# Kernel optimization log

Measured on AMD Instinct MI355X. Metric: run time of the kernel, lower is better.

Reference implementation:

```python
import jax, jax.numpy as jnp
import numpy as np

BETA = 0.9
THRESHOLD = 1.0
SLOPE = 25.0  # snntorch fast_sigmoid default slope


@jax.custom_vjp
def spike_fn(u):
    # Heaviside spike with fast-sigmoid surrogate gradient
    return (u > 0).astype(u.dtype)

def _spike_fwd(u):
    return spike_fn(u), u

def _spike_bwd(u, g):
    return (g / (SLOPE * jnp.abs(u) + 1.0) ** 2,)

spike_fn.defvjp(_spike_fwd, _spike_bwd)


def setup_inputs() -> dict:
    key = jax.random.key(0)
    k1, k2, k3 = jax.random.split(key, 3)
    T, B, D_IN, D_H = 200, 256, 512, 512
    x = jax.random.normal(k1, (T, B, D_IN), dtype=jnp.float32)
    W = jax.random.normal(k2, (D_H, D_IN), dtype=jnp.float32) * (1.0 / np.sqrt(D_IN))
    b = jax.random.normal(k3, (D_H,), dtype=jnp.float32) * 0.01
    return {"x": x, "W": W, "b": b}


def reference(x, W, b):
    # Batch the fc projection over all timesteps: [T,B,D_in] @ [D_in,D_h] -> [T,B,D_h]
    cur = jnp.einsum("tbi,hi->tbh", x, W) + b
    B, H = cur.shape[1], cur.shape[2]
    mem0 = jnp.zeros((B, H), dtype=cur.dtype)

    def step(mem, cur_t):
        # snntorch Leaky (reset_mechanism='subtract'):
        # reset from previous mem, then integrate, then fire
        reset = spike_fn(mem - THRESHOLD)
        mem_new = BETA * mem + cur_t - reset * THRESHOLD
        spk = spike_fn(mem_new - THRESHOLD)
        return mem_new, (spk, mem_new)

    _, (spk_rec, mem_rec) = jax.lax.scan(step, mem0, cur)
    return spk_rec, mem_rec
```

## Files before the change

kernel.cpp:

```cpp
#include <hip/hip_runtime.h>


#define T_STEPS 200
#define BATCH   256
#define DIN     512
#define DH      512
#define MARGIN  1e-4f
#define LISTCAP 510
#define TQ2     32

constexpr int    MM  = T_STEPS * BATCH;
constexpr int    BH  = BATCH * DH;
constexpr size_t TBH = (size_t)T_STEPS * BH;

typedef _Float16 f16x8 __attribute__((ext_vector_type(8)));
typedef _Float16 f16x4 __attribute__((ext_vector_type(4)));
typedef float    f32x4 __attribute__((ext_vector_type(4)));

constexpr size_t OFF_WH    = 104857600;
constexpr size_t OFF_WL    = 105381888;
constexpr size_t OFF_CNTB  = 105906176;
constexpr size_t OFF_LISTB = 105907200;
constexpr size_t WS_REQ    = OFF_LISTB + (size_t)256 * LISTCAP * 4;

__global__ __launch_bounds__(256) void convert_w(const float* __restrict__ W,
                                                 _Float16* __restrict__ wh,
                                                 _Float16* __restrict__ wl) {
    const int q = blockIdx.x * 256 + threadIdx.x;
    const float4 v = reinterpret_cast<const float4*>(W)[q];
    f16x4 h, l;
    h[0] = (_Float16)v.x; l[0] = (_Float16)((v.x - (float)h[0]) * 4096.0f);
    h[1] = (_Float16)v.y; l[1] = (_Float16)((v.y - (float)h[1]) * 4096.0f);
    h[2] = (_Float16)v.z; l[2] = (_Float16)((v.z - (float)h[2]) * 4096.0f);
    h[3] = (_Float16)v.w; l[3] = (_Float16)((v.w - (float)h[3]) * 4096.0f);
    const int row = q >> 7;
    const int k   = (q & 127) * 4;
    const int osw = ((k >> 3) & 3) ^ ((row >> 1) & 3);
    const long long dst = (long long)row * 512 + (k & ~31) + (osw << 3) + (k & 7);
    *reinterpret_cast<f16x4*>(wh + dst) = h;
    *reinterpret_cast<f16x4*>(wl + dst) = l;
}

__device__ __forceinline__ void gload16(const void* g, void* l) {
    __builtin_amdgcn_global_load_lds(
        (const __attribute__((address_space(1))) void*)g,
        (__attribute__((address_space(3))) void*)l, 16, 0, 0);
}

__global__ __launch_bounds__(256) void gemm_split(const float* __restrict__ x,
                                                  const _Float16* __restrict__ wh,
                                                  const _Float16* __restrict__ wl,
                                                  const float* __restrict__ bias,
                                                  float* __restrict__ C) {
    __shared__ _Float16 ldsA[2][2][128][32];
    __shared__ _Float16 ldsB[2][2][64][32];

    const int tid  = threadIdx.x;
    const int w    = tid >> 6;
    const int lane = tid & 63;
    const int wr   = (w >> 1) * 64;
    const int wc   = (w & 1) * 32;
    const int lrow = lane & 15;
    const int gsw  = (((lane >> 4) ^ ((lrow >> 1) & 3)) * 8);

    const int orig = (blockIdx.x & 7) * 400 + (blockIdx.x >> 3);
    const int row0 = (orig >> 3) * 128;
    const int col0 = (orig & 7) * 64;

    const int sr = tid >> 2;
    const int so = tid & 3;
    const int kq = so * 8;

    f32x4 acc_hh[4][2] = {};
    f32x4 acc_cr[4][2] = {};

    auto stage = [&](int bf, int k0) {
#pragma unroll
        for (int p = 0; p < 2; ++p) {
            const int r = sr + p * 64;
            const float* src = &x[(size_t)(row0 + r) * DIN + k0 + kq];
            const float4 v0 = *reinterpret_cast<const float4*>(src);
            const float4 v1 = *reinterpret_cast<const float4*>(src + 4);
            f16x8 h, l;
            h[0] = (_Float16)v0.x; l[0] = (_Float16)((v0.x - (float)h[0]) * 4096.0f);
            h[1] = (_Float16)v0.y; l[1] = (_Float16)((v0.y - (float)h[1]) * 4096.0f);
            h[2] = (_Float16)v0.z; l[2] = (_Float16)((v0.z - (float)h[2]) * 4096.0f);
            h[3] = (_Float16)v0.w; l[3] = (_Float16)((v0.w - (float)h[3]) * 4096.0f);
            h[4] = (_Float16)v1.x; l[4] = (_Float16)((v1.x - (float)h[4]) * 4096.0f);
            h[5] = (_Float16)v1.y; l[5] = (_Float16)((v1.y - (float)h[5]) * 4096.0f);
            h[6] = (_Float16)v1.z; l[6] = (_Float16)((v1.z - (float)h[6]) * 4096.0f);
            h[7] = (_Float16)v1.w; l[7] = (_Float16)((v1.w - (float)h[7]) * 4096.0f);
            const int po = (so ^ ((r >> 1) & 3)) * 8;
            *reinterpret_cast<f16x8*>(&ldsA[bf][0][r][po]) = h;
            *reinterpret_cast<f16x8*>(&ldsA[bf][1][r][po]) = l;
        }
        gload16(wh + (size_t)(col0 + sr) * DIN + k0 + kq, &ldsB[bf][0][sr][kq]);
        gload16(wl + (size_t)(col0 + sr) * DIN + k0 + kq, &ldsB[bf][1][sr][kq]);
    };

    stage(0, 0);

    int buf = 0;
    for (int kt = 0; kt < 16; ++kt) {
        __syncthreads();
        if (kt < 15) stage(buf ^ 1, (kt + 1) * 32);

        f16x8 ah[4], al[4];
#pragma unroll
        for (int fr = 0; fr < 4; ++fr) {
            ah[fr] = *reinterpret_cast<const f16x8*>(&ldsA[buf][0][wr + fr * 16 + lrow][gsw]);
            al[fr] = *reinterpret_cast<const f16x8*>(&ldsA[buf][1][wr + fr * 16 + lrow][gsw]);
        }
#pragma unroll
        for (int fc = 0; fc < 2; ++fc) {
            const f16x8 bh = *reinterpret_cast<const f16x8*>(&ldsB[buf][0][wc + fc * 16 + lrow][gsw]);
            const f16x8 bl = *reinterpret_cast<const f16x8*>(&ldsB[buf][1][wc + fc * 16 + lrow][gsw]);
#pragma unroll
            for (int fr = 0; fr < 4; ++fr) {
                acc_hh[fr][fc] = __builtin_amdgcn_mfma_f32_16x16x32_f16(ah[fr], bh, acc_hh[fr][fc], 0, 0, 0);
                acc_cr[fr][fc] = __builtin_amdgcn_mfma_f32_16x16x32_f16(ah[fr], bl, acc_cr[fr][fc], 0, 0, 0);
                acc_cr[fr][fc] = __builtin_amdgcn_mfma_f32_16x16x32_f16(al[fr], bh, acc_cr[fr][fc], 0, 0, 0);
            }
        }
        buf ^= 1;
    }

#pragma unroll
    for (int fr = 0; fr < 4; ++fr)
#pragma unroll
        for (int fc = 0; fc < 2; ++fc) {
            const int col = col0 + wc + fc * 16 + lrow;
            const float bv = bias[col];
#pragma unroll
            for (int r = 0; r < 4; ++r) {
                const int row = row0 + wr + fr * 16 + (lane >> 4) * 4 + r;
                C[(size_t)row * DH + col] =
                    acc_hh[fr][fc][r] + acc_cr[fr][fc][r] * (1.0f / 4096.0f) + bv;
            }
        }
}

__global__ __launch_bounds__(256) void snn_scan_flag(float* __restrict__ buf,
                                                     float* __restrict__ spk,
                                                     unsigned* __restrict__ cnt_b,
                                                     unsigned* __restrict__ list_b) {
#pragma clang fp contract(off)
    const int i = (blockIdx.x * 256 + threadIdx.x) * 2;
    float2 c[8];
#pragma unroll
    for (int t = 0; t < 8; ++t)
        c[t] = *reinterpret_cast<const float2*>(&buf[(size_t)t * BH + i]);
    float mem0 = 0.0f, mem1 = 0.0f;
    bool f0 = false, f1 = false;
#pragma unroll 8
    for (int t = 0; t < T_STEPS - 8; ++t) {
        const float2 cur = c[t & 7];
        c[t & 7] = *reinterpret_cast<const float2*>(&buf[(size_t)(t + 8) * BH + i]);
        const float r0 = (mem0 > 1.0f) ? 1.0f : 0.0f;
        float tmp0 = 0.9f * mem0; tmp0 = tmp0 + cur.x; mem0 = tmp0 - r0;
        f0 = f0 || (fabsf(mem0 - 1.0f) < MARGIN);
        const float r1 = (mem1 > 1.0f) ? 1.0f : 0.0f;
        float tmp1 = 0.9f * mem1; tmp1 = tmp1 + cur.y; mem1 = tmp1 - r1;
        f1 = f1 || (fabsf(mem1 - 1.0f) < MARGIN);
        float2 s, m;
        s.x = (mem0 > 1.0f) ? 1.0f : 0.0f;
        s.y = (mem1 > 1.0f) ? 1.0f : 0.0f;
        m.x = mem0; m.y = mem1;
        *reinterpret_cast<float2*>(&spk[(size_t)t * BH + i]) = s;
        *reinterpret_cast<float2*>(&buf[(size_t)t * BH + i]) = m;
    }
#pragma unroll
    for (int t = T_STEPS - 8; t < T_STEPS; ++t) {
        const float2 cur = c[t & 7];
        const float r0 = (mem0 > 1.0f) ? 1.0f : 0.0f;
        float tmp0 = 0.9f * mem0; tmp0 = tmp0 + cur.x; mem0 = tmp0 - r0;
        f0 = f0 || (fabsf(mem0 - 1.0f) < MARGIN);
        const float r1 = (mem1 > 1.0f) ? 1.0f : 0.0f;
        float tmp1 = 0.9f * mem1; tmp1 = tmp1 + cur.y; mem1 = tmp1 - r1;
        f1 = f1 || (fabsf(mem1 - 1.0f) < MARGIN);
        float2 s, m;
        s.x = (mem0 > 1.0f) ? 1.0f : 0.0f;
        s.y = (mem1 > 1.0f) ? 1.0f : 0.0f;
        m.x = mem0; m.y = mem1;
        *reinterpret_cast<float2*>(&spk[(size_t)t * BH + i]) = s;
        *reinterpret_cast<float2*>(&buf[(size_t)t * BH + i]) = m;
    }
    if (f0) {
        const int b = i >> 9;
        const unsigned slot = atomicAdd(&cnt_b[b], 1u);
        if (slot < (unsigned)LISTCAP) list_b[(size_t)b * LISTCAP + slot] = (unsigned)(i & 511);
    }
    if (f1) {
        const int b = (i + 1) >> 9;
        const unsigned slot = atomicAdd(&cnt_b[b], 1u);
        if (slot < (unsigned)LISTCAP) list_b[(size_t)b * LISTCAP + slot] = (unsigned)((i + 1) & 511);
    }
}

__global__ __launch_bounds__(256) void exact_cur_g(const float* __restrict__ x,
                                                   const float* __restrict__ W,
                                                   const float* __restrict__ bias,
                                                   const unsigned* __restrict__ cnt_b,
                                                   const unsigned* __restrict__ list_b,
                                                   float* __restrict__ cur_ex) {
    const int b = blockIdx.x;
    unsigned n = cnt_b[b];
    if (n == 0) return;
    const bool all = (n > (unsigned)LISTCAP);
    if (all) n = 512;

    const int jl = (int)(threadIdx.x & 7);
    const int tl = (int)(threadIdx.x >> 3);
    const int t  = blockIdx.y * TQ2 + tl;
    if (t >= T_STEPS) return;
    const float4* xr = reinterpret_cast<const float4*>(x + ((size_t)t * BATCH + b) * DIN);

    for (unsigned base = 0; base < n; base += 8) {
        const unsigned slot = base + (unsigned)jl;
        if (slot >= n) break;
        const int h = all ? (int)slot : (int)list_b[(size_t)b * LISTCAP + slot];
        const float4* wr = reinterpret_cast<const float4*>(W + (size_t)h * DIN);
        float acc = 0.0f;
#pragma unroll 8
        for (int kk = 0; kk < DIN / 4; ++kk) {
            const float4 a = xr[kk];
            const float4 ww = wr[kk];
            acc = fmaf(a.x, ww.x, acc);
            acc = fmaf(a.y, ww.y, acc);
            acc = fmaf(a.z, ww.z, acc);
            acc = fmaf(a.w, ww.w, acc);
        }
        cur_ex[((size_t)b * 512 + slot) * T_STEPS + t] = acc + bias[h];
    }
}

__global__ __launch_bounds__(256) void rescan_g(const float* __restrict__ cur_ex,
                                                const unsigned* __restrict__ cnt_b,
                                                const unsigned* __restrict__ list_b,
                                                float* __restrict__ buf,
                                                float* __restrict__ spk) {
#pragma clang fp contract(off)
    const int b = blockIdx.x;
    unsigned n = cnt_b[b];
    if (n == 0) return;
    const bool all = (n > (unsigned)LISTCAP);
    if (all) n = 512;

    for (unsigned slot = threadIdx.x; slot < n; slot += 256) {
        const int h = all ? (int)slot : (int)list_b[(size_t)b * LISTCAP + slot];
        const unsigned i = ((unsigned)b << 9) | (unsigned)h;
        const float* cr = cur_ex + ((size_t)b * 512 + slot) * T_STEPS;
        float mem = 0.0f;
        for (int t = 0; t < T_STEPS; ++t) {
            const float c = cr[t];
            const float reset = (mem > 1.0f) ? 1.0f : 0.0f;
            float tmp = 0.9f * mem;
            tmp = tmp + c;
            mem = tmp - reset;
            const float s = (mem > 1.0f) ? 1.0f : 0.0f;
            spk[(size_t)t * BH + i] = s;
            buf[(size_t)t * BH + i] = mem;
        }
    }
}

#define BKf 32
#define LPADf 132
__global__ __launch_bounds__(256, 3) void gemm_nt_f32(const float* __restrict__ A,
                                                      const float* __restrict__ W,
                                                      const float* __restrict__ bias,
                                                      float* __restrict__ C) {
    __shared__ float As[BKf][LPADf];
    __shared__ float Bs[BKf][LPADf];
    const int tid = threadIdx.x;
    const int tx = tid & 15, ty = tid >> 4;
    const int row0 = blockIdx.x * 128, col0 = blockIdx.y * 128;
    const int lr = tid >> 2, lk = (tid & 3) * 4;
    const float* Abase = A + (size_t)(row0 + lr) * DIN + lk;
    const float* Bbase = W + (size_t)(col0 + lr) * DIN + lk;
    float acc[8][8] = {};
    float4 ra00, ra01, ra10, ra11, rb00, rb01, rb10, rb11;
#define LOADREG(k0)                                                        \
    do {                                                                   \
        ra00 = *reinterpret_cast<const float4*>(Abase + (k0));             \
        ra01 = *reinterpret_cast<const float4*>(Abase + (k0) + 16);        \
        ra10 = *reinterpret_cast<const float4*>(Abase + 64 * DIN + (k0));  \
        ra11 = *reinterpret_cast<const float4*>(Abase + 64 * DIN + (k0) + 16); \
        rb00 = *reinterpret_cast<const float4*>(Bbase + (k0));             \
        rb01 = *reinterpret_cast<const float4*>(Bbase + (k0) + 16);        \
        rb10 = *reinterpret_cast<const float4*>(Bbase + 64 * DIN + (k0));  \
        rb11 = *reinterpret_cast<const float4*>(Bbase + 64 * DIN + (k0) + 16); \
    } while (0)
#define STOREV(arr, kb, r, v)                                              \
    do { arr[(kb)+0][r]=(v).x; arr[(kb)+1][r]=(v).y; arr[(kb)+2][r]=(v).z; arr[(kb)+3][r]=(v).w; } while (0)
    LOADREG(0);
    for (int kt = 0; kt < DIN / BKf; ++kt) {
        __syncthreads();
        STOREV(As, lk, lr, ra00); STOREV(As, 16 + lk, lr, ra01);
        STOREV(As, lk, lr + 64, ra10); STOREV(As, 16 + lk, lr + 64, ra11);
        STOREV(Bs, lk, lr, rb00); STOREV(Bs, 16 + lk, lr, rb01);
        STOREV(Bs, lk, lr + 64, rb10); STOREV(Bs, 16 + lk, lr + 64, rb11);
        __syncthreads();
        if (kt + 1 < DIN / BKf) LOADREG((kt + 1) * BKf);
#pragma unroll 8
        for (int k = 0; k < BKf; ++k) {
            float a[8], b[8];
            const float4 t0 = *reinterpret_cast<const float4*>(&As[k][ty * 8 + 0]);
            const float4 t1 = *reinterpret_cast<const float4*>(&As[k][ty * 8 + 4]);
            a[0]=t0.x; a[1]=t0.y; a[2]=t0.z; a[3]=t0.w;
            a[4]=t1.x; a[5]=t1.y; a[6]=t1.z; a[7]=t1.w;
            const float4 u0 = *reinterpret_cast<const float4*>(&Bs[k][tx * 4]);
            const float4 u1 = *reinterpret_cast<const float4*>(&Bs[k][64 + tx * 4]);
            b[0]=u0.x; b[1]=u0.y; b[2]=u0.z; b[3]=u0.w;
            b[4]=u1.x; b[5]=u1.y; b[6]=u1.z; b[7]=u1.w;
#pragma unroll
            for (int i = 0; i < 8; ++i)
#pragma unroll
                for (int j = 0; j < 8; ++j) acc[i][j] += a[i] * b[j];
        }
    }
#pragma unroll
    for (int i = 0; i < 8; ++i) {
        const int r = row0 + ty * 8 + i, c0 = col0 + tx * 4, c1 = col0 + 64 + tx * 4;
        float4 o0, o1;
        o0.x = acc[i][0] + bias[c0 + 0]; o0.y = acc[i][1] + bias[c0 + 1];
        o0.z = acc[i][2] + bias[c0 + 2]; o0.w = acc[i][3] + bias[c0 + 3];
        o1.x = acc[i][4] + bias[c1 + 0]; o1.y = acc[i][5] + bias[c1 + 1];
        o1.z = acc[i][6] + bias[c1 + 2]; o1.w = acc[i][7] + bias[c1 + 3];
        *reinterpret_cast<float4*>(&C[(size_t)r * DH + c0]) = o0;
        *reinterpret_cast<float4*>(&C[(size_t)r * DH + c1]) = o1;
    }
#undef LOADREG
#undef STOREV
}

__global__ __launch_bounds__(256) void snn_scan(float* buf, float* spk) {
    const int i = blockIdx.x * 256 + threadIdx.x;
    float mem = 0.0f;
    float c = buf[i];
    for (int t = 0; t < T_STEPS; ++t) {
        float cn = (t + 1 < T_STEPS) ? buf[(size_t)(t + 1) * BH + i] : 0.0f;
        const float reset = (mem > 1.0f) ? 1.0f : 0.0f;
        mem = 0.9f * mem + c - reset;
        const float s = (mem > 1.0f) ? 1.0f : 0.0f;
        spk[(size_t)t * BH + i] = s;
        buf[(size_t)t * BH + i] = mem;
        c = cn;
    }
}

extern "C" void kernel_launch(void* const* d_in, const int* in_sizes, int n_in,
                              void* d_out, int out_size, void* d_ws, size_t ws_size,
                              hipStream_t stream) {
    const float* x    = (const float*)d_in[0];
    const float* W    = (const float*)d_in[1];
    const float* bias = (const float*)d_in[2];
    float* out = (float*)d_out;
    float* spk = out;
    float* mem = out + TBH;

    if (ws_size >= WS_REQ) {
        char* ws = (char*)d_ws;
        _Float16* wh = (_Float16*)(ws + OFF_WH);
        _Float16* wl = (_Float16*)(ws + OFF_WL);
        unsigned* cnt_b  = (unsigned*)(ws + OFF_CNTB);
        unsigned* list_b = (unsigned*)(ws + OFF_LISTB);
        float*    cur_ex = (float*)ws;

        hipMemsetAsync(cnt_b, 0, 1024, stream);
        convert_w<<<256, 256, 0, stream>>>(W, wh, wl);
        gemm_split<<<3200, 256, 0, stream>>>(x, wh, wl, bias, mem);
        snn_scan_flag<<<BH / 512, 256, 0, stream>>>(mem, spk, cnt_b, list_b);
        dim3 egrid(BATCH, (T_STEPS + TQ2 - 1) / TQ2);
        exact_cur_g<<<egrid, 256, 0, stream>>>(x, W, bias, cnt_b, list_b, cur_ex);
        rescan_g<<<BATCH, 256, 0, stream>>>(cur_ex, cnt_b, list_b, mem, spk);
    } else {
        dim3 grid(MM / 128, DH / 128);
        gemm_nt_f32<<<grid, 256, 0, stream>>>(x, W, bias, mem);
        snn_scan<<<BH / 256, 256, 0, stream>>>(mem, spk);
    }
}
```

Baseline: 305.8 us.

## Fuse exact recompute and rescan into one per-batch kernel; nontemporal scan stores

Merges the exact fp32 current recomputation and the rescan of flagged neurons into a single kernel per batch row. Currents are staged in shared memory in chunks of 16 neurons instead of a global cur_ex buffer, which removes one launch and the global round trip. The grid shrinks from 256x7 blocks to 256 blocks, and each chunk is processed serially with barriers, so parallelism drops when many neurons are flagged. The main scan also switches its spike and membrane writes to nontemporal stores.

```diff
diff --git a/kernel.cpp b/kernel.cpp
--- a/kernel.cpp
+++ b/kernel.cpp
@@ -7,7 +7,7 @@
 #define DH      512
 #define MARGIN  1e-4f
 #define LISTCAP 510
-#define TQ2     32
+#define CHUNK   16
 
 constexpr int    MM  = T_STEPS * BATCH;
 constexpr int    BH  = BATCH * DH;
@@ -16,6 +16,7 @@
 typedef _Float16 f16x8 __attribute__((ext_vector_type(8)));
 typedef _Float16 f16x4 __attribute__((ext_vector_type(4)));
 typedef float    f32x4 __attribute__((ext_vector_type(4)));
+typedef float    f32x2 __attribute__((ext_vector_type(2)));
 
 constexpr size_t OFF_WH    = 104857600;
 constexpr size_t OFF_WL    = 105381888;
@@ -146,44 +147,44 @@
                                                      unsigned* __restrict__ list_b) {
 #pragma clang fp contract(off)
     const int i = (blockIdx.x * 256 + threadIdx.x) * 2;
-    float2 c[8];
+    f32x2 c[8];
 #pragma unroll
     for (int t = 0; t < 8; ++t)
-        c[t] = *reinterpret_cast<const float2*>(&buf[(size_t)t * BH + i]);
+        c[t] = *reinterpret_cast<const f32x2*>(&buf[(size_t)t * BH + i]);
     float mem0 = 0.0f, mem1 = 0.0f;
     bool f0 = false, f1 = false;
 #pragma unroll 8
     for (int t = 0; t < T_STEPS - 8; ++t) {
-        const float2 cur = c[t & 7];
-        c[t & 7] = *reinterpret_cast<const float2*>(&buf[(size_t)(t + 8) * BH + i]);
+        const f32x2 cur = c[t & 7];
+        c[t & 7] = *reinterpret_cast<const f32x2*>(&buf[(size_t)(t + 8) * BH + i]);
         const float r0 = (mem0 > 1.0f) ? 1.0f : 0.0f;
-        float tmp0 = 0.9f * mem0; tmp0 = tmp0 + cur.x; mem0 = tmp0 - r0;
+        float tmp0 = 0.9f * mem0; tmp0 = tmp0 + cur[0]; mem0 = tmp0 - r0;
         f0 = f0 || (fabsf(mem0 - 1.0f) < MARGIN);
         const float r1 = (mem1 > 1.0f) ? 1.0f : 0.0f;
-        float tmp1 = 0.9f * mem1; tmp1 = tmp1 + cur.y; mem1 = tmp1 - r1;
+        float tmp1 = 0.9f * mem1; tmp1 = tmp1 + cur[1]; mem1 = tmp1 - r1;
         f1 = f1 || (fabsf(mem1 - 1.0f) < MARGIN);
-        float2 s, m;
-        s.x = (mem0 > 1.0f) ? 1.0f : 0.0f;
-        s.y = (mem1 > 1.0f) ? 1.0f : 0.0f;
-        m.x = mem0; m.y = mem1;
-        *reinterpret_cast<float2*>(&spk[(size_t)t * BH + i]) = s;
-        *reinterpret_cast<float2*>(&buf[(size_t)t * BH + i]) = m;
+        f32x2 s, m;
+        s[0] = (mem0 > 1.0f) ? 1.0f : 0.0f;
+        s[1] = (mem1 > 1.0f) ? 1.0f : 0.0f;
+        m[0] = mem0; m[1] = mem1;
+        __builtin_nontemporal_store(s, reinterpret_cast<f32x2*>(&spk[(size_t)t * BH + i]));
+        __builtin_nontemporal_store(m, reinterpret_cast<f32x2*>(&buf[(size_t)t * BH + i]));
     }
 #pragma unroll
     for (int t = T_STEPS - 8; t < T_STEPS; ++t) {
-        const float2 cur = c[t & 7];
+        const f32x2 cur = c[t & 7];
         const float r0 = (mem0 > 1.0f) ? 1.0f : 0.0f;
-        float tmp0 = 0.9f * mem0; tmp0 = tmp0 + cur.x; mem0 = tmp0 - r0;
+        float tmp0 = 0.9f * mem0; tmp0 = tmp0 + cur[0]; mem0 = tmp0 - r0;
         f0 = f0 || (fabsf(mem0 - 1.0f) < MARGIN);
         const float r1 = (mem1 > 1.0f) ? 1.0f : 0.0f;
-        float tmp1 = 0.9f * mem1; tmp1 = tmp1 + cur.y; mem1 = tmp1 - r1;
+        float tmp1 = 0.9f * mem1; tmp1 = tmp1 + cur[1]; mem1 = tmp1 - r1;
         f1 = f1 || (fabsf(mem1 - 1.0f) < MARGIN);
-        float2 s, m;
-        s.x = (mem0 > 1.0f) ? 1.0f : 0.0f;
-        s.y = (mem1 > 1.0f) ? 1.0f : 0.0f;
-        m.x = mem0; m.y = mem1;
-        *reinterpret_cast<float2*>(&spk[(size_t)t * BH + i]) = s;
-        *reinterpret_cast<float2*>(&buf[(size_t)t * BH + i]) = m;
+        f32x2 s, m;
+        s[0] = (mem0 > 1.0f) ? 1.0f : 0.0f;
+        s[1] = (mem1 > 1.0f) ? 1.0f : 0.0f;
+        m[0] = mem0; m[1] = mem1;
+        __builtin_nontemporal_store(s, reinterpret_cast<f32x2*>(&spk[(size_t)t * BH + i]));
+        __builtin_nontemporal_store(m, reinterpret_cast<f32x2*>(&buf[(size_t)t * BH + i]));
     }
     if (f0) {
         const int b = i >> 9;
@@ -197,70 +198,73 @@
     }
 }
 
-__global__ __launch_bounds__(256) void exact_cur_g(const float* __restrict__ x,
-                                                   const float* __restrict__ W,
-                                                   const float* __restrict__ bias,
-                                                   const unsigned* __restrict__ cnt_b,
-                                                   const unsigned* __restrict__ list_b,
-                                                   float* __restrict__ cur_ex) {
+__global__ __launch_bounds__(256) void exact_group2(const float* __restrict__ x,
+                                                    const float* __restrict__ W,
+                                                    const float* __restrict__ bias,
+                                                    const unsigned* __restrict__ cnt_b,
+                                                    const unsigned* __restrict__ list_b,
+                                                    float* __restrict__ buf,
+                                                    float* __restrict__ spk) {
     const int b = blockIdx.x;
     unsigned n = cnt_b[b];
     if (n == 0) return;
     const bool all = (n > (unsigned)LISTCAP);
     if (all) n = 512;
 
+    __shared__ float curL[CHUNK][T_STEPS];
+    __shared__ int   hsel[CHUNK];
+
     const int jl = (int)(threadIdx.x & 7);
     const int tl = (int)(threadIdx.x >> 3);
-    const int t  = blockIdx.y * TQ2 + tl;
-    if (t >= T_STEPS) return;
-    const float4* xr = reinterpret_cast<const float4*>(x + ((size_t)t * BATCH + b) * DIN);
-
-    for (unsigned base = 0; base < n; base += 8) {
-        const unsigned slot = base + (unsigned)jl;
-        if (slot >= n) break;
-        const int h = all ? (int)slot : (int)list_b[(size_t)b * LISTCAP + slot];
-        const float4* wr = reinterpret_cast<const float4*>(W + (size_t)h * DIN);
-        float acc = 0.0f;
+
+    for (unsigned base = 0; base < n; base += CHUNK) {
+        const int cn = (int)((n - base < CHUNK) ? (n - base) : CHUNK);
+        if (threadIdx.x < (unsigned)cn)
+            hsel[threadIdx.x] = all ? (int)(base + threadIdx.x)
+                                    : (int)list_b[(size_t)b * LISTCAP + base + threadIdx.x];
+        __syncthreads();
+
+#pragma unroll
+        for (int j8 = 0; j8 < CHUNK; j8 += 8) {
+            const int j = j8 + jl;
+            if (j < cn) {
+                const int h = hsel[j];
+                const float4* wr = reinterpret_cast<const float4*>(W + (size_t)h * DIN);
+                for (int t = tl; t < T_STEPS; t += 32) {
+                    const float4* xr = reinterpret_cast<const float4*>(x + ((size_t)t * BATCH + b) * DIN);
+                    float acc = 0.0f;
 #pragma unroll 8
-        for (int kk = 0; kk < DIN / 4; ++kk) {
-            const float4 a = xr[kk];
-            const float4 ww = wr[kk];
-            acc = fmaf(a.x, ww.x, acc);
-            acc = fmaf(a.y, ww.y, acc);
-            acc = fmaf(a.z, ww.z, acc);
-            acc = fmaf(a.w, ww.w, acc);
-        }
-        cur_ex[((size_t)b * 512 + slot) * T_STEPS + t] = acc + bias[h];
-    }
-}
-
-__global__ __launch_bounds__(256) void rescan_g(const float* __restrict__ cur_ex,
-                                                const unsigned* __restrict__ cnt_b,
-                                                const unsigned* __restrict__ list_b,
-                                                float* __restrict__ buf,
-                                                float* __restrict__ spk) {
+                    for (int kk = 0; kk < DIN / 4; ++kk) {
+                        const float4 a = xr[kk];
+                        const float4 ww = wr[kk];
+                        acc = fmaf(a.x, ww.x, acc);
+                        acc = fmaf(a.y, ww.y, acc);
+                        acc = fmaf(a.z, ww.z, acc);
+                        acc = fmaf(a.w, ww.w, acc);
+                    }
+                    curL[j][t] = acc + bias[h];
+                }
+            }
+        }
+        __syncthreads();
+
+        if (threadIdx.x < (unsigned)cn) {
 #pragma clang fp contract(off)
-    const int b = blockIdx.x;
-    unsigned n = cnt_b[b];
-    if (n == 0) return;
-    const bool all = (n > (unsigned)LISTCAP);
-    if (all) n = 512;
-
-    for (unsigned slot = threadIdx.x; slot < n; slot += 256) {
-        const int h = all ? (int)slot : (int)list_b[(size_t)b * LISTCAP + slot];
-        const unsigned i = ((unsigned)b << 9) | (unsigned)h;
-        const float* cr = cur_ex + ((size_t)b * 512 + slot) * T_STEPS;
-        float mem = 0.0f;
-        for (int t = 0; t < T_STEPS; ++t) {
-            const float c = cr[t];
-            const float reset = (mem > 1.0f) ? 1.0f : 0.0f;
-            float tmp = 0.9f * mem;
-            tmp = tmp + c;
-            mem = tmp - reset;
-            const float s = (mem > 1.0f) ? 1.0f : 0.0f;
-            spk[(size_t)t * BH + i] = s;
-            buf[(size_t)t * BH + i] = mem;
-        }
+            const int j = threadIdx.x;
+            const unsigned i = ((unsigned)b << 9) | (unsigned)hsel[j];
+            float mem = 0.0f;
+            for (int t = 0; t < T_STEPS; ++t) {
+                const float c = curL[j][t];
+                const float reset = (mem > 1.0f) ? 1.0f : 0.0f;
+                float tmp = 0.9f * mem;
+                tmp = tmp + c;
+                mem = tmp - reset;
+                const float s = (mem > 1.0f) ? 1.0f : 0.0f;
+                spk[(size_t)t * BH + i] = s;
+                buf[(size_t)t * BH + i] = mem;
+            }
+        }
+        __syncthreads();
     }
 }
 
@@ -365,15 +369,12 @@
         _Float16* wl = (_Float16*)(ws + OFF_WL);
         unsigned* cnt_b  = (unsigned*)(ws + OFF_CNTB);
         unsigned* list_b = (unsigned*)(ws + OFF_LISTB);
-        float*    cur_ex = (float*)ws;
-
-        hipMemsetAsync(cnt_b, 0, 1024, stream);
+
+        (void)hipMemsetAsync(cnt_b, 0, 1024, stream);
         convert_w<<<256, 256, 0, stream>>>(W, wh, wl);
         gemm_split<<<3200, 256, 0, stream>>>(x, wh, wl, bias, mem);
         snn_scan_flag<<<BH / 512, 256, 0, stream>>>(mem, spk, cnt_b, list_b);
-        dim3 egrid(BATCH, (T_STEPS + TQ2 - 1) / TQ2);
-        exact_cur_g<<<egrid, 256, 0, stream>>>(x, W, bias, cnt_b, list_b, cur_ex);
-        rescan_g<<<BATCH, 256, 0, stream>>>(cur_ex, cnt_b, list_b, mem, spk);
+        exact_group2<<<BATCH, 256, 0, stream>>>(x, W, bias, cnt_b, list_b, mem, spk);
     } else {
         dim3 grid(MM / 128, DH / 128);
         gemm_nt_f32<<<grid, 256, 0, stream>>>(x, W, bias, mem);
```

Result: slower. 312.4 us (+2.1%).
